# Optimization experiments

Hardware: AMD Instinct MI355X
Metric: run time of the kernel (lower is better)

## Reference

```python
import jax, jax.numpy as jnp
import numpy as np

NUM_USERS = 100000
NUM_ITEMS = 100000
EMB = 64
N_LAYERS = 3
N_FOLD = 2
NNZ_PER_FOLD = 1600000
LEAKY_ALPHA = 0.2  # tf.nn.leaky_relu default


def setup_inputs() -> dict:
    key = jax.random.key(0)
    ks = jax.random.split(key, 8)
    scale = 1.0 / np.sqrt(EMB)
    return {
        "user_table": jax.random.normal(ks[0], (NUM_USERS, EMB), jnp.float32) * scale,
        "item_table": jax.random.normal(ks[1], (NUM_ITEMS, EMB), jnp.float32) * scale,
        "W1": jax.random.normal(ks[2], (N_LAYERS, EMB, EMB), jnp.float32) * scale,
        "W2": jax.random.normal(ks[3], (N_LAYERS, EMB, EMB), jnp.float32) * scale,
        "adj_vals": jax.random.uniform(ks[4], (N_FOLD, NNZ_PER_FOLD), jnp.float32),
        "adj_rows": jax.random.randint(ks[5], (N_FOLD, NNZ_PER_FOLD), 0, NUM_USERS + NUM_ITEMS, jnp.int32),
        "adj_cols": jax.random.randint(ks[6], (N_FOLD, NNZ_PER_FOLD), 0, NUM_USERS + NUM_ITEMS, jnp.int32),
        "user_indices": jnp.arange(NUM_USERS, dtype=jnp.int32),
        "item_indices": jnp.arange(NUM_ITEMS, dtype=jnp.int32),
    }


def reference(user_table, item_table, W1, W2, adj_vals, adj_rows, adj_cols, user_indices, item_indices):
    u0 = user_table[user_indices]          # [Nu, D]
    i0 = item_table[item_indices]          # [Ni, D]
    nu = u0.shape[0]
    all_emb = jnp.concatenate([u0, i0], axis=0)   # [Nt, D]
    n_total = all_emb.shape[0]
    all_u = [u0]
    all_i = [i0]
    n_layers = W1.shape[0]
    n_fold = adj_rows.shape[0]
    for l in range(n_layers):
        layer_emb = jnp.zeros_like(all_emb)
        for f in range(n_fold):
            # SpMM: relevant = A_fold @ all_emb  (COO scatter-add)
            gathered = all_emb[adj_cols[f]] * adj_vals[f][:, None]     # [nnz, D]
            relevant = jax.ops.segment_sum(gathered, adj_rows[f], num_segments=n_total)
            # dual dense projections + elementwise gate, summed
            layer_emb = layer_emb + relevant @ W1[l] + (relevant * all_emb) @ W2[l]
        all_emb = jax.nn.leaky_relu(layer_emb, negative_slope=LEAKY_ALPHA)
        all_u.append(all_emb[:nu])
        all_i.append(all_emb[nu:])
    final_u = jnp.concatenate(all_u, axis=1)   # [Nu, D*(L+1)]
    final_i = jnp.concatenate(all_i, axis=1)   # [Ni, D*(L+1)]
    return jnp.sum(final_u * final_i, axis=1)  # [Nu]
```

## Files before the change

### kernel.cpp

```cpp
#include <hip/hip_runtime.h>

#define NU 100000
#define NT 200000
#define D 64
#define NLAYERS 3
#define NNZ_TOTAL 3200000
#define ALPHA 0.2f
#define NBUCKET 391
#define BSHIFT 9
#define CHUNK 4096

typedef unsigned short ushort_t;
typedef __attribute__((ext_vector_type(8))) short bf16x8;
typedef __attribute__((ext_vector_type(4))) float f32x4;

__device__ __forceinline__ float bf2f(ushort_t h) {
    return __uint_as_float((unsigned)h << 16);
}
__device__ __forceinline__ ushort_t f2bf(float x) {
    unsigned u = __float_as_uint(x);
    u += 0x7FFF + ((u >> 16) & 1);
    return (ushort_t)(u >> 16);
}

__global__ __launch_bounds__(256) void init_dot_kernel(
    const float* __restrict__ ut, const float* __restrict__ it,
    const int* __restrict__ uidx, const int* __restrict__ iidx,
    ushort_t* __restrict__ E, float* __restrict__ out)
{
    int w = (blockIdx.x * 256 + threadIdx.x) >> 6;
    int lane = threadIdx.x & 63;
    if (w >= NU) return;
    float eu = ut[uidx[w] * D + lane];
    float ei = it[iidx[w] * D + lane];
    E[w * D + lane] = f2bf(eu);
    E[(NU + w) * D + lane] = f2bf(ei);
    float p = eu * ei;
#pragma unroll
    for (int off = 32; off > 0; off >>= 1) p += __shfl_xor(p, off);
    if (lane == 0) out[w] = p;
}

__global__ __launch_bounds__(256) void bucket_hist_kernel(const int* __restrict__ rows,
                                                          int* __restrict__ bcnt)
{
    __shared__ int l[NBUCKET];
    int t = threadIdx.x;
    for (int k = t; k < NBUCKET; k += 256) l[k] = 0;
    __syncthreads();
    int base = blockIdx.x * CHUNK;
#pragma unroll
    for (int q = 0; q < 16; ++q) {
        int i = base + q * 256 + t;
        if (i < NNZ_TOTAL) atomicAdd(&l[rows[i] >> BSHIFT], 1);
    }
    __syncthreads();
    for (int k = t; k < NBUCKET; k += 256) if (l[k]) atomicAdd(&bcnt[k], l[k]);
}

__global__ __launch_bounds__(512) void scan_buckets_kernel(const int* __restrict__ bcnt,
                                                           int* __restrict__ bstart,
                                                           int* __restrict__ bcur)
{
    __shared__ int s[512];
    int t = threadIdx.x;
    int v = (t < NBUCKET) ? bcnt[t] : 0;
    s[t] = v; __syncthreads();
    for (int off = 1; off < 512; off <<= 1) {
        int x = (t >= off) ? s[t - off] : 0;
        __syncthreads();
        s[t] += x;
        __syncthreads();
    }
    if (t < NBUCKET) { bstart[t] = s[t] - v; bcur[t] = s[t] - v; }
    if (t == 511) bstart[NBUCKET] = s[511];
}

__global__ __launch_bounds__(256) void bin_kernel(
    const int* __restrict__ rows, const int* __restrict__ cols,
    const float* __restrict__ vals, int* __restrict__ bcur,
    int2* __restrict__ binned)
{
    __shared__ int lcount[NBUCKET];
    __shared__ int lbase[NBUCKET];
    int t = threadIdx.x;
    for (int k = t; k < NBUCKET; k += 256) lcount[k] = 0;
    __syncthreads();
    int base = blockIdx.x * CHUNK;
    int pk[16];
#pragma unroll
    for (int q = 0; q < 16; ++q) {
        int i = base + q * 256 + t;
        pk[q] = 0;
        if (i < NNZ_TOTAL) {
            int r = rows[i];
            int b = r >> BSHIFT;
            int rank = atomicAdd(&lcount[b], 1);
            pk[q] = (b << 22) | (rank << 10) | (r & 511);
        }
    }
    __syncthreads();
    for (int k = t; k < NBUCKET; k += 256)
        if (lcount[k]) lbase[k] = atomicAdd(&bcur[k], lcount[k]);
    __syncthreads();
#pragma unroll
    for (int q = 0; q < 16; ++q) {
        int i = base + q * 256 + t;
        if (i < NNZ_TOTAL) {
            int b    = (pk[q] >> 22) & 0x1FF;
            int rank = (pk[q] >> 10) & 0xFFF;
            int rl   =  pk[q] & 0x1FF;
            binned[lbase[b] + rank] =
                make_int2((rl << 18) | cols[i], __float_as_int(vals[i]));
        }
    }
}

__global__ __launch_bounds__(256) void scatter2_kernel(
    const int2* __restrict__ binned, const int* __restrict__ bstart,
    int* __restrict__ row_ptr, int2* __restrict__ csr)
{
    __shared__ int lbuf[512];
    __shared__ int aux[256];
    int b = blockIdx.x, t = threadIdx.x;
    int rowbase = b << BSHIFT;
    int nrows = min(512, NT - rowbase);
    int beg = bstart[b], end = bstart[b + 1];
    for (int k = t; k < 512; k += 256) lbuf[k] = 0;
    __syncthreads();
    for (int i = beg + t; i < end; i += 256)
        atomicAdd(&lbuf[binned[i].x >> 18], 1);
    __syncthreads();
    int c0 = lbuf[t * 2], c1 = lbuf[t * 2 + 1];
    int s = c0 + c1;
    aux[t] = s; __syncthreads();
    for (int off = 1; off < 256; off <<= 1) {
        int x = (t >= off) ? aux[t - off] : 0;
        __syncthreads();
        aux[t] += x;
        __syncthreads();
    }
    int p0 = beg + aux[t] - s;
    int p1 = p0 + c0;
    lbuf[t * 2] = p0; lbuf[t * 2 + 1] = p1;
    if (t * 2     < nrows) row_ptr[rowbase + t * 2]     = p0;
    if (t * 2 + 1 < nrows) row_ptr[rowbase + t * 2 + 1] = p1;
    if (t == 0) row_ptr[rowbase + nrows] = end;
    __syncthreads();
    for (int i = beg + t; i < end; i += 256) {
        int2 p = binned[i];
        int pos = atomicAdd(&lbuf[p.x >> 18], 1);
        csr[pos] = make_int2(p.x & 0x3FFFF, p.y);
    }
}

__global__ __launch_bounds__(256) void spmm_kernel(
    const ushort_t* __restrict__ E, const int* __restrict__ row_ptr,
    const int2* __restrict__ csr, ushort_t* __restrict__ R)
{
    int w = (blockIdx.x * 256 + threadIdx.x) >> 6;
    int lane = threadIdx.x & 63;
    if (w >= NT) return;
    int beg = __builtin_amdgcn_readfirstlane(row_ptr[w]);
    int end = __builtin_amdgcn_readfirstlane(row_ptr[w + 1]);
    float acc = 0.f;
    for (int j = beg; j < end; j += 16) {
        int2 p[16];
#pragma unroll
        for (int q = 0; q < 16; ++q) p[q] = csr[j + q];
        float ev[16];
#pragma unroll
        for (int q = 0; q < 16; ++q) {
            bool ok = (j + q) < end;
            int col = ok ? p[q].x : 0;
            ev[q] = bf2f(E[col * D + lane]);
        }
#pragma unroll
        for (int q = 0; q < 16; ++q) {
            float v = ((j + q) < end) ? __int_as_float(p[q].y) : 0.f;
            acc += v * ev[q];
        }
    }
    R[w * D + lane] = f2bf(acc);
}

__global__ __launch_bounds__(256) void mfma_dense_kernel(
    const ushort_t* __restrict__ R, ushort_t* E,
    const float* __restrict__ W1, const float* __restrict__ W2)
{
    __shared__ __align__(16) ushort_t Bt[2][64 * 128];
    int t = threadIdx.x;
    for (int idx = t; idx < 4096; idx += 256) {
        int k = idx >> 6, n = idx & 63;
        float w1 = W1[idx], w2 = W2[idx];
        ushort_t h1 = f2bf(w1); ushort_t l1 = f2bf(w1 - bf2f(h1));
        ushort_t h2 = f2bf(w2); ushort_t l2 = f2bf(w2 - bf2f(h2));
        int sw1 = (k >> 3) ^ (n & 15);
        Bt[0][n * 128 + sw1 * 8 + (k & 7)] = h1;
        Bt[1][n * 128 + sw1 * 8 + (k & 7)] = l1;
        int k2 = k + 64;
        int sw2 = (k2 >> 3) ^ (n & 15);
        Bt[0][n * 128 + sw2 * 8 + (k2 & 7)] = h2;
        Bt[1][n * 128 + sw2 * 8 + (k2 & 7)] = l2;
    }
    __syncthreads();
    int lane = t & 63, wl = t >> 6;
    int sub = lane >> 4, l15 = lane & 15;
    for (int chunk = blockIdx.x; chunk < NT / 64; chunk += gridDim.x) {
        int row = chunk * 64 + wl * 16 + l15;
        const bf16x8* Rrow = (const bf16x8*)(R + row * 64);
        const bf16x8* Erow = (const bf16x8*)(E + row * 64);
        bf16x8 a0 = Rrow[sub];
        bf16x8 a1 = Rrow[4 + sub];
        bf16x8 e0 = Erow[sub];
        bf16x8 e1 = Erow[4 + sub];
        bf16x8 a2, a3;
#pragma unroll
        for (int j = 0; j < 8; ++j) {
            a2[j] = (short)f2bf(bf2f((ushort_t)a0[j]) * bf2f((ushort_t)e0[j]));
            a3[j] = (short)f2bf(bf2f((ushort_t)a1[j]) * bf2f((ushort_t)e1[j]));
        }
        bf16x8 afrag[4] = {a0, a1, a2, a3};
        f32x4 acc[4];
#pragma unroll
        for (int n0 = 0; n0 < 4; ++n0) acc[n0] = (f32x4){0.f, 0.f, 0.f, 0.f};
#pragma unroll
        for (int n0 = 0; n0 < 4; ++n0) {
            int n = n0 * 16 + l15;
#pragma unroll
            for (int ks = 0; ks < 4; ++ks) {
                int sw = (ks * 4 + sub) ^ (n & 15);
                bf16x8 bh = *(const bf16x8*)&Bt[0][n * 128 + sw * 8];
                bf16x8 bl = *(const bf16x8*)&Bt[1][n * 128 + sw * 8];
                acc[n0] = __builtin_amdgcn_mfma_f32_16x16x32_bf16(afrag[ks], bh, acc[n0], 0, 0, 0);
                acc[n0] = __builtin_amdgcn_mfma_f32_16x16x32_bf16(afrag[ks], bl, acc[n0], 0, 0, 0);
            }
        }
        int rowbase = chunk * 64 + wl * 16 + sub * 4;
#pragma unroll
        for (int n0 = 0; n0 < 4; ++n0) {
#pragma unroll
            for (int reg = 0; reg < 4; ++reg) {
                float o = acc[n0][reg];
                o = o > 0.f ? o : ALPHA * o;
                E[(rowbase + reg) * 64 + n0 * 16 + l15] = f2bf(o);
            }
        }
    }
}

__global__ __launch_bounds__(256) void dot_kernel(const ushort_t* __restrict__ E,
                                                  float* __restrict__ out)
{
    int w = (blockIdx.x * 256 + threadIdx.x) >> 6;
    int lane = threadIdx.x & 63;
    if (w >= NU) return;
    float p = bf2f(E[w * D + lane]) * bf2f(E[(NU + w) * D + lane]);
#pragma unroll
    for (int off = 32; off > 0; off >>= 1) p += __shfl_xor(p, off);
    if (lane == 0) out[w] += p;
}

extern "C" void kernel_launch(void* const* d_in, const int* in_sizes, int n_in,
                              void* d_out, int out_size, void* d_ws, size_t ws_size,
                              hipStream_t stream)
{
    const float* ut   = (const float*)d_in[0];
    const float* it   = (const float*)d_in[1];
    const float* W1   = (const float*)d_in[2];
    const float* W2   = (const float*)d_in[3];
    const float* vals = (const float*)d_in[4];
    const int*   rows = (const int*)d_in[5];
    const int*   cols = (const int*)d_in[6];
    const int*   uidx = (const int*)d_in[7];
    const int*   iidx = (const int*)d_in[8];
    float* out = (float*)d_out;

    char* ws = (char*)d_ws;
    ushort_t* E    = (ushort_t*)(ws + 0);
    ushort_t* R    = (ushort_t*)(ws + 25600000);
    int2*  binned  = (int2*) (ws + 25600000);
    int*   row_ptr = (int*)  (ws + 51200000);
    int*   bcnt    = (int*)  (ws + 52000256);
    int*   bstart  = (int*)  (ws + 52002304);
    int*   bcur    = (int*)  (ws + 52004352);
    int2*  csr     = (int2*) (ws + 52006400);

    hipMemsetAsync(bcnt, 0, NBUCKET * 4, stream);

    init_dot_kernel<<<NU / 4, 256, 0, stream>>>(ut, it, uidx, iidx, E, out);

    const int NBLK = (NNZ_TOTAL + CHUNK - 1) / CHUNK;
    bucket_hist_kernel<<<NBLK, 256, 0, stream>>>(rows, bcnt);
    scan_buckets_kernel<<<1, 512, 0, stream>>>(bcnt, bstart, bcur);
    bin_kernel<<<NBLK, 256, 0, stream>>>(rows, cols, vals, bcur, binned);
    scatter2_kernel<<<NBUCKET, 256, 0, stream>>>(binned, bstart, row_ptr, csr);

    for (int l = 0; l < NLAYERS; ++l) {
        spmm_kernel<<<NT / 4, 256, 0, stream>>>(E, row_ptr, csr, R);
        mfma_dense_kernel<<<1024, 256, 0, stream>>>(R, E, W1 + l * 4096, W2 + l * 4096);
        dot_kernel<<<NU / 4, 256, 0, stream>>>(E, out);
    }
}
```

Baseline: 627.9 us.

## Replace global atomic bucket offsets with per-block count matrix and scan

The binning pass now writes per-block bucket histograms to a count matrix, scans it per bucket, and gives each block deterministic write offsets instead of reserving ranges with global atomics. This drops the memset and the global atomic contention, and makes element order within each bucket deterministic. The chunk size is halved so more blocks run. In exchange it adds a scan kernel and an extra count buffer in the workspace.

```diff
diff --git a/kernel.cpp b/kernel.cpp
--- a/kernel.cpp
+++ b/kernel.cpp
@@ -8,7 +8,8 @@
 #define ALPHA 0.2f
 #define NBUCKET 391
 #define BSHIFT 9
-#define CHUNK 4096
+#define CHUNK 2048
+#define NBLK_C 1563
 
 typedef unsigned short ushort_t;
 typedef __attribute__((ext_vector_type(8))) short bf16x8;
@@ -41,26 +42,49 @@
     if (lane == 0) out[w] = p;
 }
 
-__global__ __launch_bounds__(256) void bucket_hist_kernel(const int* __restrict__ rows,
-                                                          int* __restrict__ bcnt)
+__global__ __launch_bounds__(256) void count_kernel(const int* __restrict__ rows,
+                                                    int* __restrict__ cnt)
 {
     __shared__ int l[NBUCKET];
-    int t = threadIdx.x;
+    int t = threadIdx.x, b = blockIdx.x;
     for (int k = t; k < NBUCKET; k += 256) l[k] = 0;
     __syncthreads();
-    int base = blockIdx.x * CHUNK;
-#pragma unroll
-    for (int q = 0; q < 16; ++q) {
+    int base = b * CHUNK;
+#pragma unroll
+    for (int q = 0; q < 8; ++q) {
         int i = base + q * 256 + t;
         if (i < NNZ_TOTAL) atomicAdd(&l[rows[i] >> BSHIFT], 1);
     }
     __syncthreads();
-    for (int k = t; k < NBUCKET; k += 256) if (l[k]) atomicAdd(&bcnt[k], l[k]);
+    for (int k = t; k < NBUCKET; k += 256) cnt[k * NBLK_C + b] = l[k];
+}
+
+__global__ __launch_bounds__(256) void scan_cnt_kernel(int* __restrict__ cnt,
+                                                       int* __restrict__ bcnt)
+{
+    __shared__ int s[256];
+    int k = blockIdx.x, t = threadIdx.x;
+    int carry = 0;
+    for (int base = 0; base < NBLK_C; base += 256) {
+        int idx = base + t;
+        int v = (idx < NBLK_C) ? cnt[k * NBLK_C + idx] : 0;
+        s[t] = v; __syncthreads();
+        for (int off = 1; off < 256; off <<= 1) {
+            int x = (t >= off) ? s[t - off] : 0;
+            __syncthreads();
+            s[t] += x;
+            __syncthreads();
+        }
+        int ex = s[t] - v + carry;
+        if (idx < NBLK_C) cnt[k * NBLK_C + idx] = ex;
+        carry += s[255];
+        __syncthreads();
+    }
+    if (t == 0) bcnt[k] = carry;
 }
 
 __global__ __launch_bounds__(512) void scan_buckets_kernel(const int* __restrict__ bcnt,
-                                                           int* __restrict__ bstart,
-                                                           int* __restrict__ bcur)
+                                                           int* __restrict__ bstart)
 {
     __shared__ int s[512];
     int t = threadIdx.x;
@@ -72,45 +96,44 @@
         s[t] += x;
         __syncthreads();
     }
-    if (t < NBUCKET) { bstart[t] = s[t] - v; bcur[t] = s[t] - v; }
+    if (t < NBUCKET) bstart[t] = s[t] - v;
     if (t == 511) bstart[NBUCKET] = s[511];
 }
 
 __global__ __launch_bounds__(256) void bin_kernel(
     const int* __restrict__ rows, const int* __restrict__ cols,
-    const float* __restrict__ vals, int* __restrict__ bcur,
-    int2* __restrict__ binned)
+    const float* __restrict__ vals, const int* __restrict__ cnt,
+    const int* __restrict__ bstart, int2* __restrict__ binned)
 {
     __shared__ int lcount[NBUCKET];
     __shared__ int lbase[NBUCKET];
-    int t = threadIdx.x;
-    for (int k = t; k < NBUCKET; k += 256) lcount[k] = 0;
-    __syncthreads();
-    int base = blockIdx.x * CHUNK;
-    int pk[16];
-#pragma unroll
-    for (int q = 0; q < 16; ++q) {
+    int t = threadIdx.x, b = blockIdx.x;
+    for (int k = t; k < NBUCKET; k += 256) {
+        lcount[k] = 0;
+        lbase[k] = bstart[k] + cnt[k * NBLK_C + b];
+    }
+    __syncthreads();
+    int base = b * CHUNK;
+    int pk[8];
+#pragma unroll
+    for (int q = 0; q < 8; ++q) {
         int i = base + q * 256 + t;
         pk[q] = 0;
         if (i < NNZ_TOTAL) {
             int r = rows[i];
-            int b = r >> BSHIFT;
-            int rank = atomicAdd(&lcount[b], 1);
-            pk[q] = (b << 22) | (rank << 10) | (r & 511);
-        }
-    }
-    __syncthreads();
-    for (int k = t; k < NBUCKET; k += 256)
-        if (lcount[k]) lbase[k] = atomicAdd(&bcur[k], lcount[k]);
-    __syncthreads();
-#pragma unroll
-    for (int q = 0; q < 16; ++q) {
+            int bk = r >> BSHIFT;
+            int rank = atomicAdd(&lcount[bk], 1);
+            pk[q] = (bk << 20) | (rank << 9) | (r & 511);
+        }
+    }
+#pragma unroll
+    for (int q = 0; q < 8; ++q) {
         int i = base + q * 256 + t;
         if (i < NNZ_TOTAL) {
-            int b    = (pk[q] >> 22) & 0x1FF;
-            int rank = (pk[q] >> 10) & 0xFFF;
+            int bk   = (pk[q] >> 20) & 0x1FF;
+            int rank = (pk[q] >> 9) & 0x7FF;
             int rl   =  pk[q] & 0x1FF;
-            binned[lbase[b] + rank] =
+            binned[lbase[bk] + rank] =
                 make_int2((rl << 18) | cols[i], __float_as_int(vals[i]));
         }
     }
@@ -283,17 +306,15 @@
     int*   row_ptr = (int*)  (ws + 51200000);
     int*   bcnt    = (int*)  (ws + 52000256);
     int*   bstart  = (int*)  (ws + 52002304);
-    int*   bcur    = (int*)  (ws + 52004352);
-    int2*  csr     = (int2*) (ws + 52006400);
-
-    hipMemsetAsync(bcnt, 0, NBUCKET * 4, stream);
+    int2*  csr     = (int2*) (ws + 52004352);
+    int*   cnt     = (int*)  (ws + 77604352);
 
     init_dot_kernel<<<NU / 4, 256, 0, stream>>>(ut, it, uidx, iidx, E, out);
 
-    const int NBLK = (NNZ_TOTAL + CHUNK - 1) / CHUNK;
-    bucket_hist_kernel<<<NBLK, 256, 0, stream>>>(rows, bcnt);
-    scan_buckets_kernel<<<1, 512, 0, stream>>>(bcnt, bstart, bcur);
-    bin_kernel<<<NBLK, 256, 0, stream>>>(rows, cols, vals, bcur, binned);
+    count_kernel<<<NBLK_C, 256, 0, stream>>>(rows, cnt);
+    scan_cnt_kernel<<<NBUCKET, 256, 0, stream>>>(cnt, bcnt);
+    scan_buckets_kernel<<<1, 512, 0, stream>>>(bcnt, bstart);
+    bin_kernel<<<NBLK_C, 256, 0, stream>>>(rows, cols, vals, cnt, bstart, binned);
     scatter2_kernel<<<NBUCKET, 256, 0, stream>>>(binned, bstart, row_ptr, csr);
 
     for (int l = 0; l < NLAYERS; ++l) {
```

Result: faster. 605.5 us (-3.6%).
